# Performance work log

Hardware: AMD Instinct MI355X
Metric: run time of the kernel (lower is better)

Reference implementation:

```python
import jax, jax.numpy as jnp
import numpy as np

NUM_FRAMES = 8
NUM_HEADS = 12
NEG = -1e9


def _masks(N):
    i = jnp.arange(N)[:, None]
    j = jnp.arange(N)[None, :]
    b = NUM_FRAMES + 1  # boundary = 9
    head = (i < b) & (j < b)
    body = ((i >= b) & (j >= b)) | ((i == 0) & (j >= b)) | ((i >= b) & (j == 0)) | ((i == 0) & (j == 0))
    interact = ((i >= b) & (j < b)) | ((i < b) & (j >= b)) | ((i == 0) & (j == 0))
    return head, body, interact


def setup_inputs() -> dict:
    key = jax.random.key(0)
    k1, k2, k3 = jax.random.split(key, 3)
    B, N, C = 8, 1024, 768
    x = jax.random.normal(k1, (B, N, C), dtype=jnp.float32)
    w_qkv = jax.random.normal(k2, (3 * C, C), dtype=jnp.float32) * 0.02
    w_proj = jax.random.normal(k3, (C, C), dtype=jnp.float32) * 0.02
    b_proj = jnp.zeros((C,), dtype=jnp.float32)
    return {"x": x, "w_qkv": w_qkv, "w_proj": w_proj, "b_proj": b_proj}


def reference(x, w_qkv, w_proj, b_proj):
    B, N, C = x.shape
    H = NUM_HEADS
    hd = C // H
    scale = hd ** (-0.5)

    qkv = (x @ w_qkv.T).reshape(B, N, 3, H, hd).transpose(2, 0, 3, 1, 4)  # [3,B,H,N,hd]
    q, k, v = qkv[0], qkv[1], qkv[2]

    attn = jnp.einsum("bhnd,bhmd->bhnm", q, k) * scale  # [B,H,N,N]

    head_m, body_m, inter_m = _masks(N)

    def branch(mask):
        scores = jnp.where(mask, attn, NEG)
        p = jax.nn.softmax(scores, axis=-1)
        o = jnp.einsum("bhnm,bhmd->bhnd", p, v)  # [B,H,N,hd]
        o = o.transpose(0, 2, 1, 3).reshape(B, N, C)
        return o @ w_proj.T + b_proj

    return branch(head_m), branch(body_m), branch(inter_m)
```

## Files before the change

### kernel.cpp

```cpp
#include <hip/hip_runtime.h>
#include <stdint.h>

typedef unsigned short u16;
typedef unsigned int u32;
using f32x4 = __attribute__((ext_vector_type(4))) float;
using bf16x8 = __attribute__((ext_vector_type(8))) short;
using u16x8 = __attribute__((ext_vector_type(8))) unsigned short;
using u16x4 = __attribute__((ext_vector_type(4))) unsigned short;
using u32x2 = __attribute__((ext_vector_type(2))) unsigned int;

#define QSCALE 0.18033688f

__device__ __forceinline__ u16 f2bf(float f) {
  u32 u = __float_as_uint(f);
  u32 r = (u + 0x7FFFu + ((u >> 16) & 1u)) >> 16;
  return (u16)r;
}
__device__ __forceinline__ float bf2f(u16 h) { return __uint_as_float(((u32)h) << 16); }

__device__ __forceinline__ float fexp2(float x) { return __builtin_amdgcn_exp2f(x); }

__device__ __forceinline__ u32 pack_trunc(float lo, float hi) {
  return __builtin_amdgcn_perm(__float_as_uint(hi), __float_as_uint(lo), 0x07060302u);
}

__device__ __forceinline__ void gload16(const void* g, void* l) {
  __builtin_amdgcn_global_load_lds((const __attribute__((address_space(1))) void*)g,
                                   (__attribute__((address_space(3))) void*)l, 16, 0, 0);
}

__global__ __launch_bounds__(256) void cvt3_kernel(const float* __restrict__ a, u16* __restrict__ da, int n4a,
                                                   const float* __restrict__ b, u16* __restrict__ db, int n4b,
                                                   const float* __restrict__ c, u16* __restrict__ dc, int n4c,
                                                   int n4sb) {
  int i = blockIdx.x * 256 + threadIdx.x;
  const float* src;
  u16* dst;
  int n;
  float s = 1.0f;
  if (i < n4a) {
    src = a; dst = da; n = i;
  } else if (i < n4a + n4b) {
    src = b; dst = db; n = i - n4a;
    if (n < n4sb) s = QSCALE;
  } else if (i < n4a + n4b + n4c) {
    src = c; dst = dc; n = i - n4a - n4b;
  } else {
    return;
  }
  const float4 f = ((const float4*)src)[n];
  u16x4 o;
  o[0] = f2bf(f.x * s); o[1] = f2bf(f.y * s); o[2] = f2bf(f.z * s); o[3] = f2bf(f.w * s);
  ((u16x4*)dst)[n] = o;
}

template <int MODE, int Mdim, int Ndim, int Kdim>
__global__ __launch_bounds__(256) void gemm_bt(const u16* __restrict__ A, const u16* __restrict__ Bw,
                                               u16* __restrict__ qb, u16* __restrict__ kb,
                                               u16* __restrict__ vTb,
                                               float* __restrict__ out, const float* __restrict__ bias) {
  __shared__ __align__(16) u16 lA[2][128 * 32];
  __shared__ __align__(16) u16 lB[2][128 * 32];
  const int tid = threadIdx.x;
  const int wid = tid >> 6, lane = tid & 63;
  int m0;
  if constexpr (MODE == 1) {
    const int mb = blockIdx.x;
    m0 = (mb < 128) ? (8192 + mb * 128) : ((mb - 128) * 1024);
  } else {
    m0 = blockIdx.x * 128;
  }
  const int n0 = blockIdx.y * 128;
  const int wm = (wid >> 1) * 64, wn = (wid & 1) * 64;
  const int g = lane >> 4, r16 = lane & 15;

  f32x4 acc[4][4] = {};

  const int srow = wid * 16 + (lane >> 2);
  const int scol = (lane & 3) * 8;
  const u16* gA = A + (size_t)(m0 + srow) * Kdim + scol;
  const u16* gB = Bw + (size_t)(n0 + srow) * Kdim + scol;

  gload16(gA, lA[0] + wid * 512);
  gload16(gA + (size_t)64 * Kdim, lA[0] + wid * 512 + 2048);
  gload16(gB, lB[0] + wid * 512);
  gload16(gB + (size_t)64 * Kdim, lB[0] + wid * 512 + 2048);
  __syncthreads();

  int cur = 0;
  for (int k0 = 0; k0 < Kdim; k0 += 32) {
    if (k0 + 32 < Kdim) {
      const int nk = k0 + 32;
      u16* lAn = lA[cur ^ 1] + wid * 512;
      u16* lBn = lB[cur ^ 1] + wid * 512;
      gload16(gA + nk, lAn);
      gload16(gA + (size_t)64 * Kdim + nk, lAn + 2048);
      gload16(gB + nk, lBn);
      gload16(gB + (size_t)64 * Kdim + nk, lBn + 2048);
    }
    const u16* lAc = lA[cur];
    const u16* lBc = lB[cur];
    bf16x8 af[4], bfr[4];
#pragma unroll
    for (int i = 0; i < 4; ++i) af[i] = *(const bf16x8*)(lAc + (wm + i * 16 + r16) * 32 + g * 8);
#pragma unroll
    for (int j = 0; j < 4; ++j) bfr[j] = *(const bf16x8*)(lBc + (wn + j * 16 + r16) * 32 + g * 8);
#pragma unroll
    for (int i = 0; i < 4; ++i)
#pragma unroll
      for (int j = 0; j < 4; ++j)
        acc[i][j] = __builtin_amdgcn_mfma_f32_16x16x32_bf16(af[i], bfr[j], acc[i][j], 0, 0, 0);
    __syncthreads();
    cur ^= 1;
  }

#pragma unroll
  for (int i = 0; i < 4; ++i) {
    const int gm = m0 + wm + i * 16 + g * 4;
#pragma unroll
    for (int j = 0; j < 4; ++j) {
      const int gn = n0 + wn + j * 16 + r16;
      if constexpr (MODE == 1) {
        const float bv = bias[gn];
#pragma unroll
        for (int r = 0; r < 4; ++r) out[(size_t)(gm + r) * Ndim + gn] = acc[i][j][r] + bv;
      } else {
        const int t = gn / 768;
        const int rem = gn - t * 768;
        const int h = rem >> 6, d = rem & 63;
        if (t == 2) {
          u16x4 pk;
#pragma unroll
          for (int r = 0; r < 4; ++r) pk[r] = f2bf(acc[i][j][r]);
          const int b = gm >> 10, n = gm & 1023;
          *(u16x4*)(vTb + ((size_t)((b * 12 + h) * 64 + d)) * 1024 + n) = pk;
        } else {
          u16* dst = (t == 0) ? qb : kb;
#pragma unroll
          for (int r = 0; r < 4; ++r) {
            const int b = (gm + r) >> 10, n = (gm + r) & 1023;
            dst[((size_t)((b * 12 + h) * 1024 + n)) * 64 + d] = f2bf(acc[i][j][r]);
          }
        }
      }
    }
  }
}

__global__ __launch_bounds__(192) void bcast_fill(float* __restrict__ out) {
  const int row = blockIdx.x;
  const int b = row / 896;
  const int r = row - b * 896;
  const size_t src = (size_t)(b * 1024 + 9) * 768;
  const size_t dst = (size_t)(b * 1024 + 128 + r) * 768;
  const float4 v = ((const float4*)(out + src))[threadIdx.x];
  ((float4*)(out + dst))[threadIdx.x] = v;
}

__global__ __launch_bounds__(256) void vmean_kernel(const u16* __restrict__ vTb,
                                                    float* __restrict__ vmean) {
  const int bh = blockIdx.x, t = threadIdx.x;
  const int d = t >> 2, part = t & 3;
  const u16* src = vTb + ((size_t)bh * 64 + d) * 1024 + part * 256;
  float s = 0.f;
  for (int j = 0; j < 256; j += 8) {
    u16x8 u = *(const u16x8*)(src + j);
#pragma unroll
    for (int e = 0; e < 8; ++e) s += bf2f(u[e]);
  }
  s += __shfl_xor(s, 1);
  s += __shfl_xor(s, 2);
  if (part == 0) vmean[bh * 64 + d] = s * (1.0f / 1024.0f);
}

__global__ __launch_bounds__(256) void body_attn(const u16* __restrict__ qg, const u16* __restrict__ kg,
                                                 const u16* __restrict__ vg, const float* __restrict__ vmean,
                                                 u16* __restrict__ og) {
  __shared__ __align__(16) u16 lK[2][64 * 64];
  __shared__ __align__(16) u16 lV[2][64 * 64];
  __shared__ __align__(16) u16 lP[4][16 * 72];

  const int blk = blockIdx.x;
  const int gid = (blk & 7) * 192 + (blk >> 3);
  const int rt = gid & 15, bh = gid >> 4;
  const int tid = threadIdx.x, wid = tid >> 6, lane = tid & 63;
  const int g = lane >> 4, r16 = lane & 15;
  const int row0 = rt * 64 + wid * 16;

  const u16* qrow = qg + ((size_t)bh * 1024 + row0 + r16) * 64;
  const bf16x8 aq0 = *(const bf16x8*)(qrow + g * 8);
  const bf16x8 aq1 = *(const bf16x8*)(qrow + 32 + g * 8);

  const int lrow = lane >> 3, lch = lane & 7;
  const int swz = (lch ^ lrow) * 8;
  const int j0 = wid * 2;
  const u16* gK = kg + (size_t)bh * 65536 + (size_t)(j0 * 8 + lrow) * 64 + swz;
  const u16* gV = vg + (size_t)bh * 65536 + (size_t)(j0 * 8 + lrow) * 1024 + swz;

  f32x4 oa[4] = {};
  f32x4 osum = {};
  u16* lPw = lP[wid];

  bf16x8 vones;
#pragma unroll
  for (int i = 0; i < 8; ++i) vones[i] = (short)0x3F80;

  auto stage = [&](int c0, int buf) {
    gload16(gK + (size_t)c0 * 64, lK[buf] + j0 * 512);
    gload16(gK + (size_t)c0 * 64 + 512, lK[buf] + (j0 + 1) * 512);
    gload16(gV + c0, lV[buf] + j0 * 512);
    gload16(gV + c0 + 8192, lV[buf] + (j0 + 1) * 512);
  };

  auto compute = [&](const u16* lKc, const u16* lVc, int c0) {
#pragma unroll
    for (int kt = 0; kt < 4; ++kt) {
      const int key = kt * 16 + r16;
      const bf16x8 bk0 = *(const bf16x8*)(lKc + key * 64 + ((g ^ (key & 7)) * 8));
      const bf16x8 bk1 = *(const bf16x8*)(lKc + key * 64 + (((4 + g) ^ (key & 7)) * 8));
      f32x4 S = {};
      S = __builtin_amdgcn_mfma_f32_16x16x32_bf16(bk0, aq0, S, 0, 0, 0);
      S = __builtin_amdgcn_mfma_f32_16x16x32_bf16(bk1, aq1, S, 0, 0, 0);
      float p[4];
#pragma unroll
      for (int r = 0; r < 4; ++r) p[r] = fexp2(S[r]);
      if (c0 == 0 && kt == 0) {
        const int q = row0 + r16;
        const bool dropk0 = (q >= 1 && q <= 8);
#pragma unroll
        for (int r = 0; r < 4; ++r) {
          const int k = 4 * g + r;
          const bool keep = (k >= 9) || (k == 0 && !dropk0);
          p[r] = keep ? p[r] : 0.f;
        }
      }
      u32x2 w;
      w[0] = pack_trunc(p[0], p[1]);
      w[1] = pack_trunc(p[2], p[3]);
      *(u32x2*)((char*)lPw + r16 * 144 + kt * 32 + g * 8) = w;
    }
#pragma unroll
    for (int m = 0; m < 2; ++m) {
      const bf16x8 ap = *(const bf16x8*)((char*)lPw + r16 * 144 + m * 64 + g * 16);
#pragma unroll
      for (int jt = 0; jt < 4; ++jt) {
        const int d = jt * 16 + r16;
        const bf16x8 bv = *(const bf16x8*)(lVc + d * 64 + (((m * 4 + g) ^ (d & 7)) * 8));
        oa[jt] = __builtin_amdgcn_mfma_f32_16x16x32_bf16(ap, bv, oa[jt], 0, 0, 0);
      }
      osum = __builtin_amdgcn_mfma_f32_16x16x32_bf16(ap, vones, osum, 0, 0, 0);
    }
  };

  stage(0, 0);
  __syncthreads();

  for (int it = 0; it < 8; ++it) {
    const int c0 = it * 128;
    stage(c0 + 64, 1);
    compute(lK[0], lV[0], c0);
    __syncthreads();
    if (it < 7) stage(c0 + 128, 0);
    compute(lK[1], lV[1], c0 + 64);
    __syncthreads();
  }

  const int b = bh / 12, h = bh - b * 12;
#pragma unroll
  for (int r = 0; r < 4; ++r) {
    const int grow = row0 + 4 * g + r;
    const bool full = (grow >= 1 && grow <= 8);
    const float inv = 1.f / osum[r];
#pragma unroll
    for (int jt = 0; jt < 4; ++jt) {
      const int d = jt * 16 + r16;
      const float vi = oa[jt][r] * inv;
      const float vb = full ? vmean[bh * 64 + d] : vi;
      og[((size_t)(8192 + b * 1024 + grow)) * 768 + h * 64 + d] = f2bf(vb);
      if (grow <= 8)
        og[((size_t)(16384 + b * 1024 + grow)) * 768 + h * 64 + d] = f2bf(vi);
    }
  }
}

__global__ __launch_bounds__(256) void smalls_attn(const u16* __restrict__ qg, const u16* __restrict__ kg,
                                                   const u16* __restrict__ vg, const float* __restrict__ vmean,
                                                   u16* __restrict__ og) {
  __shared__ __align__(16) u16 lP2[4][16 * 40];
  __shared__ float lsRed[4][16];
  const int bh = blockIdx.y;
  const int b = bh / 12, h = bh - b * 12;
  const int tid = threadIdx.x, wid = tid >> 6, lane = tid & 63;
  const int g = lane >> 4, r16 = lane & 15;
  u16* lPw = lP2[wid];

  const int row0 = blockIdx.x * 64 + wid * 16;
  const u16* qrow = qg + ((size_t)bh * 1024 + row0 + r16) * 64;
  const bf16x8 aq0 = *(const bf16x8*)(qrow + g * 8);
  const bf16x8 aq1 = *(const bf16x8*)(qrow + 32 + g * 8);
  const u16* krow = kg + ((size_t)bh * 1024 + r16) * 64;
  const bf16x8 bk0 = *(const bf16x8*)(krow + g * 8);
  const bf16x8 bk1 = *(const bf16x8*)(krow + 32 + g * 8);
  f32x4 S = {};
  S = __builtin_amdgcn_mfma_f32_16x16x32_bf16(bk0, aq0, S, 0, 0, 0);
  S = __builtin_amdgcn_mfma_f32_16x16x32_bf16(bk1, aq1, S, 0, 0, 0);
  float p[4];
  float lsum = 0.f;
#pragma unroll
  for (int r = 0; r < 4; ++r) {
    const int k = 4 * g + r;
    p[r] = (k < 9) ? fexp2(S[r]) : 0.f;
    lsum += p[r];
  }
  {
    u16x4 pk;
#pragma unroll
    for (int r = 0; r < 4; ++r) pk[r] = f2bf(p[r]);
    *(u16x4*)((char*)lPw + r16 * 80 + g * 8) = pk;
    u16x4 z = {0, 0, 0, 0};
    *(u16x4*)((char*)lPw + r16 * 80 + 32 + g * 8) = z;
  }
  lsum += __shfl_xor(lsum, 16);
  lsum += __shfl_xor(lsum, 32);
  if (lane < 16) lsRed[wid][lane] = lsum;
  const bf16x8 ap = *(const bf16x8*)((char*)lPw + r16 * 80 + g * 16);
  f32x4 oa[4] = {};
#pragma unroll
  for (int jt = 0; jt < 4; ++jt) {
    const u16* vrow = vg + ((size_t)bh * 64 + jt * 16 + r16) * 1024;
    const bf16x8 bv = *(const bf16x8*)(vrow + g * 8);
    oa[jt] = __builtin_amdgcn_mfma_f32_16x16x32_bf16(ap, bv, oa[jt], 0, 0, 0);
  }
#pragma unroll
  for (int r = 0; r < 4; ++r) {
    const int grow = row0 + 4 * g + r;
    const float inv = 1.f / lsRed[wid][4 * g + r];
#pragma unroll
    for (int jt = 0; jt < 4; ++jt) {
      const int d = jt * 16 + r16;
      const float v = oa[jt][r] * inv;
      if (grow >= 9) {
        og[((size_t)(16384 + b * 1024 + grow)) * 768 + h * 64 + d] = f2bf(v);
        og[((size_t)(b * 1024 + grow)) * 768 + h * 64 + d] = f2bf(vmean[bh * 64 + d]);
      } else {
        og[((size_t)(b * 1024 + grow)) * 768 + h * 64 + d] = f2bf(v);
      }
    }
  }
}

extern "C" void kernel_launch(void* const* d_in, const int* in_sizes, int n_in,
                              void* d_out, int out_size, void* d_ws, size_t ws_size,
                              hipStream_t stream) {
  (void)in_sizes; (void)n_in; (void)out_size; (void)ws_size;
  const float* x      = (const float*)d_in[0];
  const float* w_qkv  = (const float*)d_in[1];
  const float* w_proj = (const float*)d_in[2];
  const float* b_proj = (const float*)d_in[3];

  char* ws = (char*)d_ws;
  u16* xb     = (u16*)(ws + 0);
  u16* wqkvb  = (u16*)(ws + 12582912);
  u16* wprojb = (u16*)(ws + 16121856);
  u16* qb     = (u16*)(ws + 17301504);
  u16* kb     = (u16*)(ws + 29884416);
  u16* vTb    = (u16*)(ws + 42467328);
  float* vmn  = (float*)(ws + 55050240);
  u16* ob     = (u16*)(ws + 55074816);

  cvt3_kernel<<<8449, 256, 0, stream>>>(x, xb, 1572864, w_qkv, wqkvb, 442368,
                                        w_proj, wprojb, 147456, 147456);

  gemm_bt<0, 8192, 2304, 768><<<dim3(64, 18), 256, 0, stream>>>(
      xb, wqkvb, qb, kb, vTb, nullptr, nullptr);

  vmean_kernel<<<96, 256, 0, stream>>>(vTb, vmn);

  body_attn<<<1536, 256, 0, stream>>>(qb, kb, vTb, vmn, ob);
  smalls_attn<<<dim3(16, 96), 256, 0, stream>>>(qb, kb, vTb, vmn, ob);

  gemm_bt<1, 24576, 768, 768><<<dim3(136, 6), 256, 0, stream>>>(
      ob, wprojb, nullptr, nullptr, nullptr, (float*)d_out, b_proj);

  bcast_fill<<<7168, 192, 0, stream>>>((float*)d_out);
}
```

Measured before the change: 169.7 us.

## Process two 64-row query tiles per block in body attention to reuse K/V tiles

Result: faster. 161.0 us (-5.1%).

```diff
diff --git a/kernel.cpp b/kernel.cpp
--- a/kernel.cpp
+++ b/kernel.cpp
@@ -178,18 +178,23 @@
                                                  u16* __restrict__ og) {
   __shared__ __align__(16) u16 lK[2][64 * 64];
   __shared__ __align__(16) u16 lV[2][64 * 64];
-  __shared__ __align__(16) u16 lP[4][16 * 72];
+  __shared__ __align__(16) u16 lPA[4][16 * 72];
+  __shared__ __align__(16) u16 lPB[4][16 * 72];
 
   const int blk = blockIdx.x;
-  const int gid = (blk & 7) * 192 + (blk >> 3);
-  const int rt = gid & 15, bh = gid >> 4;
+  const int gid = (blk & 7) * 96 + (blk >> 3);
+  const int rt2 = gid & 7, bh = gid >> 3;
   const int tid = threadIdx.x, wid = tid >> 6, lane = tid & 63;
   const int g = lane >> 4, r16 = lane & 15;
-  const int row0 = rt * 64 + wid * 16;
-
-  const u16* qrow = qg + ((size_t)bh * 1024 + row0 + r16) * 64;
-  const bf16x8 aq0 = *(const bf16x8*)(qrow + g * 8);
-  const bf16x8 aq1 = *(const bf16x8*)(qrow + 32 + g * 8);
+  const int rowA = rt2 * 128 + wid * 16;
+  const int rowB = rowA + 64;
+
+  const u16* qrowA = qg + ((size_t)bh * 1024 + rowA + r16) * 64;
+  const u16* qrowB = qg + ((size_t)bh * 1024 + rowB + r16) * 64;
+  const bf16x8 aqA0 = *(const bf16x8*)(qrowA + g * 8);
+  const bf16x8 aqA1 = *(const bf16x8*)(qrowA + 32 + g * 8);
+  const bf16x8 aqB0 = *(const bf16x8*)(qrowB + g * 8);
+  const bf16x8 aqB1 = *(const bf16x8*)(qrowB + 32 + g * 8);
 
   const int lrow = lane >> 3, lch = lane & 7;
   const int swz = (lch ^ lrow) * 8;
@@ -197,9 +202,10 @@
   const u16* gK = kg + (size_t)bh * 65536 + (size_t)(j0 * 8 + lrow) * 64 + swz;
   const u16* gV = vg + (size_t)bh * 65536 + (size_t)(j0 * 8 + lrow) * 1024 + swz;
 
-  f32x4 oa[4] = {};
-  f32x4 osum = {};
-  u16* lPw = lP[wid];
+  f32x4 oaA[4] = {}, oaB[4] = {};
+  f32x4 osumA = {}, osumB = {};
+  u16* lPAw = lPA[wid];
+  u16* lPBw = lPB[wid];
 
   bf16x8 vones;
 #pragma unroll
@@ -218,37 +224,47 @@
       const int key = kt * 16 + r16;
       const bf16x8 bk0 = *(const bf16x8*)(lKc + key * 64 + ((g ^ (key & 7)) * 8));
       const bf16x8 bk1 = *(const bf16x8*)(lKc + key * 64 + (((4 + g) ^ (key & 7)) * 8));
-      f32x4 S = {};
-      S = __builtin_amdgcn_mfma_f32_16x16x32_bf16(bk0, aq0, S, 0, 0, 0);
-      S = __builtin_amdgcn_mfma_f32_16x16x32_bf16(bk1, aq1, S, 0, 0, 0);
-      float p[4];
-#pragma unroll
-      for (int r = 0; r < 4; ++r) p[r] = fexp2(S[r]);
+      f32x4 SA = {}, SB = {};
+      SA = __builtin_amdgcn_mfma_f32_16x16x32_bf16(bk0, aqA0, SA, 0, 0, 0);
+      SA = __builtin_amdgcn_mfma_f32_16x16x32_bf16(bk1, aqA1, SA, 0, 0, 0);
+      SB = __builtin_amdgcn_mfma_f32_16x16x32_bf16(bk0, aqB0, SB, 0, 0, 0);
+      SB = __builtin_amdgcn_mfma_f32_16x16x32_bf16(bk1, aqB1, SB, 0, 0, 0);
+      float pA[4], pB[4];
+#pragma unroll
+      for (int r = 0; r < 4; ++r) { pA[r] = fexp2(SA[r]); pB[r] = fexp2(SB[r]); }
       if (c0 == 0 && kt == 0) {
-        const int q = row0 + r16;
-        const bool dropk0 = (q >= 1 && q <= 8);
+        const int qA = rowA + r16;
+        const int qB = rowB + r16;
+        const bool dropA = (qA >= 1 && qA <= 8);
+        const bool dropB = (qB >= 1 && qB <= 8);
 #pragma unroll
         for (int r = 0; r < 4; ++r) {
           const int k = 4 * g + r;
-          const bool keep = (k >= 9) || (k == 0 && !dropk0);
-          p[r] = keep ? p[r] : 0.f;
+          pA[r] = ((k >= 9) || (k == 0 && !dropA)) ? pA[r] : 0.f;
+          pB[r] = ((k >= 9) || (k == 0 && !dropB)) ? pB[r] : 0.f;
         }
       }
-      u32x2 w;
-      w[0] = pack_trunc(p[0], p[1]);
-      w[1] = pack_trunc(p[2], p[3]);
-      *(u32x2*)((char*)lPw + r16 * 144 + kt * 32 + g * 8) = w;
+      u32x2 wA, wB;
+      wA[0] = pack_trunc(pA[0], pA[1]);
+      wA[1] = pack_trunc(pA[2], pA[3]);
+      wB[0] = pack_trunc(pB[0], pB[1]);
+      wB[1] = pack_trunc(pB[2], pB[3]);
+      *(u32x2*)((char*)lPAw + r16 * 144 + kt * 32 + g * 8) = wA;
+      *(u32x2*)((char*)lPBw + r16 * 144 + kt * 32 + g * 8) = wB;
     }
 #pragma unroll
     for (int m = 0; m < 2; ++m) {
-      const bf16x8 ap = *(const bf16x8*)((char*)lPw + r16 * 144 + m * 64 + g * 16);
+      const bf16x8 apA = *(const bf16x8*)((char*)lPAw + r16 * 144 + m * 64 + g * 16);
+      const bf16x8 apB = *(const bf16x8*)((char*)lPBw + r16 * 144 + m * 64 + g * 16);
 #pragma unroll
       for (int jt = 0; jt < 4; ++jt) {
         const int d = jt * 16 + r16;
         const bf16x8 bv = *(const bf16x8*)(lVc + d * 64 + (((m * 4 + g) ^ (d & 7)) * 8));
-        oa[jt] = __builtin_amdgcn_mfma_f32_16x16x32_bf16(ap, bv, oa[jt], 0, 0, 0);
-      }
-      osum = __builtin_amdgcn_mfma_f32_16x16x32_bf16(ap, vones, osum, 0, 0, 0);
+        oaA[jt] = __builtin_amdgcn_mfma_f32_16x16x32_bf16(apA, bv, oaA[jt], 0, 0, 0);
+        oaB[jt] = __builtin_amdgcn_mfma_f32_16x16x32_bf16(apB, bv, oaB[jt], 0, 0, 0);
+      }
+      osumA = __builtin_amdgcn_mfma_f32_16x16x32_bf16(apA, vones, osumA, 0, 0, 0);
+      osumB = __builtin_amdgcn_mfma_f32_16x16x32_bf16(apB, vones, osumB, 0, 0, 0);
     }
   };
 
@@ -268,17 +284,28 @@
   const int b = bh / 12, h = bh - b * 12;
 #pragma unroll
   for (int r = 0; r < 4; ++r) {
-    const int grow = row0 + 4 * g + r;
-    const bool full = (grow >= 1 && grow <= 8);
-    const float inv = 1.f / osum[r];
-#pragma unroll
-    for (int jt = 0; jt < 4; ++jt) {
-      const int d = jt * 16 + r16;
-      const float vi = oa[jt][r] * inv;
-      const float vb = full ? vmean[bh * 64 + d] : vi;
-      og[((size_t)(8192 + b * 1024 + grow)) * 768 + h * 64 + d] = f2bf(vb);
-      if (grow <= 8)
-        og[((size_t)(16384 + b * 1024 + grow)) * 768 + h * 64 + d] = f2bf(vi);
+    {
+      const int grow = rowA + 4 * g + r;
+      const bool full = (grow >= 1 && grow <= 8);
+      const float inv = 1.f / osumA[r];
+#pragma unroll
+      for (int jt = 0; jt < 4; ++jt) {
+        const int d = jt * 16 + r16;
+        const float vi = oaA[jt][r] * inv;
+        const float vb = full ? vmean[bh * 64 + d] : vi;
+        og[((size_t)(8192 + b * 1024 + grow)) * 768 + h * 64 + d] = f2bf(vb);
+        if (grow <= 8)
+          og[((size_t)(16384 + b * 1024 + grow)) * 768 + h * 64 + d] = f2bf(vi);
+      }
+    }
+    {
+      const int grow = rowB + 4 * g + r;
+      const float inv = 1.f / osumB[r];
+#pragma unroll
+      for (int jt = 0; jt < 4; ++jt) {
+        const int d = jt * 16 + r16;
+        og[((size_t)(8192 + b * 1024 + grow)) * 768 + h * 64 + d] = f2bf(oaB[jt][r] * inv);
+      }
     }
   }
 }
@@ -376,7 +403,7 @@
 
   vmean_kernel<<<96, 256, 0, stream>>>(vTb, vmn);
 
-  body_attn<<<1536, 256, 0, stream>>>(qb, kb, vTb, vmn, ob);
+  body_attn<<<768, 256, 0, stream>>>(qb, kb, vTb, vmn, ob);
   smalls_attn<<<dim3(16, 96), 256, 0, stream>>>(qb, kb, vTb, vmn, ob);
 
   gemm_bt<1, 24576, 768, 768><<<dim3(136, 6), 256, 0, stream>>>(
```
